# Optimization experiments

Measured on AMD Instinct MI355X. Metric: run time of the kernel, lower is better.

Reference implementation:

```python
import jax, jax.numpy as jnp
from jax import lax
import numpy as np

NA, NC = 3, 1
CONF_THRESH, IOU_THRESH = 0.5, 0.5


def _conv(x, w, b, pad):
    y = lax.conv_general_dilated(x, w, (1, 1), [(pad, pad), (pad, pad)],
                                 dimension_numbers=('NCHW', 'OIHW', 'NCHW'))
    return y + b[None, :, None, None]


def _maxpool2(x):
    return lax.reduce_window(x, -jnp.inf, lax.max, (1, 1, 2, 2), (1, 1, 2, 2), 'VALID')


def _stream(x, w1, b1, w2, b2):
    x = _maxpool2(jax.nn.relu(_conv(x, w1, b1, 1)))
    x = _maxpool2(jax.nn.relu(_conv(x, w2, b2, 1)))
    return x


def _pairwise_iou(b):
    # b: [N,4] in (x1,y1,x2,y2); matches torchvision box_iou (no area clamp)
    x1, y1, x2, y2 = b[:, 0], b[:, 1], b[:, 2], b[:, 3]
    area = (x2 - x1) * (y2 - y1)
    ix1 = jnp.maximum(x1[:, None], x1[None, :])
    iy1 = jnp.maximum(y1[:, None], y1[None, :])
    ix2 = jnp.minimum(x2[:, None], x2[None, :])
    iy2 = jnp.minimum(y2[:, None], y2[None, :])
    inter = jnp.clip(ix2 - ix1, 0.0) * jnp.clip(iy2 - iy1, 0.0)
    return inter / (area[:, None] + area[None, :] - inter)


def _nms_keep(boxes, scores, conf_keep, iou_thresh):
    # Greedy NMS over a fixed, small N; returns bool keep mask (conf + NMS).
    n = boxes.shape[0]
    order = jnp.argsort(-jnp.where(conf_keep, scores, -jnp.inf))
    iou = _pairwise_iou(boxes[order])  # [N,N] in score order
    idx = jnp.arange(n)

    def body(i, state):
        keep, suppressed = state
        valid = jnp.logical_not(suppressed[i])
        keep = keep.at[i].set(valid)
        suppressed = suppressed | (valid & (iou[i] > iou_thresh) & (idx > i))
        return keep, suppressed

    keep_sorted, _ = lax.fori_loop(0, n, body,
                                   (jnp.zeros(n, bool), jnp.zeros(n, bool)))
    keep = jnp.zeros(n, bool).at[order].set(keep_sorted)
    return keep & conf_keep


def setup_inputs() -> dict:
    key = jax.random.key(0)
    ks = jax.random.split(key, 14)
    s = 0.05
    inp = {
        'x': jax.random.normal(ks[0], (8, 3, 512, 512), jnp.float32),
        'rgb_w1': jax.random.normal(ks[1], (32, 3, 3, 3), jnp.float32) * s,
        'rgb_b1': jnp.zeros((32,), jnp.float32),
        'rgb_w2': jax.random.normal(ks[2], (64, 32, 3, 3), jnp.float32) * s,
        'rgb_b2': jnp.zeros((64,), jnp.float32),
        'ir_w1': jax.random.normal(ks[3], (32, 3, 3, 3), jnp.float32) * s,
        'ir_b1': jnp.zeros((32,), jnp.float32),
        'ir_w2': jax.random.normal(ks[4], (64, 32, 3, 3), jnp.float32) * s,
        'ir_b2': jnp.zeros((64,), jnp.float32),
        'fuse_w': jax.random.normal(ks[5], (128, 128, 3, 3), jnp.float32) * s,
        'fuse_b': jnp.zeros((128,), jnp.float32),
        'det_w': jax.random.normal(ks[6], (NA * (5 + NC), 128, 1, 1), jnp.float32),
        'det_b': jax.random.normal(ks[7], (NA * (5 + NC),), jnp.float32),
    }
    return inp


def reference(x, rgb_w1, rgb_b1, rgb_w2, rgb_b2,
              ir_w1, ir_b1, ir_w2, ir_b2,
              fuse_w, fuse_b, det_w, det_b):
    f1 = _stream(x, rgb_w1, rgb_b1, rgb_w2, rgb_b2)   # [B,64,H/4,W/4]
    f2 = _stream(x, ir_w1, ir_b1, ir_w2, ir_b2)       # [B,64,H/4,W/4]
    f = jnp.concatenate([f1, f2], axis=1)             # [B,128,H/4,W/4]
    f = jax.nn.relu(_conv(f, fuse_w, fuse_b, 1))
    f = jnp.mean(f, axis=(2, 3), keepdims=True)       # AdaptiveAvgPool2d((1,1))
    p = _conv(f, det_w, det_b, 0)                     # [B,18,1,1]
    B, C, H, W = p.shape
    p = p.reshape(B, NA, 5 + NC, H, W).transpose(0, 1, 3, 4, 2)  # [B,na,H,W,5+nc]
    boxes = p[..., :4].reshape(B, -1, 4)              # [B, na*H*W, 4]
    scores = jax.nn.sigmoid(p[..., 4]).reshape(B, -1) # [B, na*H*W]
    conf_keep = scores > CONF_THRESH
    keep = jax.vmap(_nms_keep, in_axes=(0, 0, 0, None))(boxes, scores, conf_keep,
                                                        IOU_THRESH)
    # Fixed-shape equivalent of the per-image variable-length preds list:
    # preds[b] == boxes[b][keep[b]].
    return p, boxes, scores, keep
```

## Files before the change

kernel.cpp:

```cpp
#include <hip/hip_runtime.h>
#include <math.h>


typedef __bf16 bf16x8 __attribute__((ext_vector_type(8)));
typedef float f32x4 __attribute__((ext_vector_type(4)));

static __device__ __forceinline__ ushort f2bf(float f) {
    unsigned u = __float_as_uint(f);
    unsigned r = (u + 0x7fffu + ((u >> 16) & 1u)) >> 16;
    return (ushort)r;
}
static __device__ __forceinline__ float bf2f(ushort h) {
    return __uint_as_float(((unsigned)h) << 16);
}

__global__ __launch_bounds__(256) void w1prep(
    const float* __restrict__ w_rgb, const float* __restrict__ w_ir,
    uint* __restrict__ W1p)
{
    int i = blockIdx.x * 256 + threadIdx.x;
    if (i >= 2048) return;
    int s = i >> 10, r = i & 1023;
    int oc = r >> 5, k = r & 31;
    const float* w = s ? w_ir : w_rgb;
    float v = (k < 27) ? w[oc * 27 + k] : 0.f;
    ushort h = f2bf(v);
    W1p[i] = (uint)h | ((uint)f2bf(v - bf2f(h)) << 16);
}

__global__ __launch_bounds__(256) void conv1_mfma(
    const float* __restrict__ x, const uint* __restrict__ W1p,
    const float* __restrict__ bias, ushort* __restrict__ C1h,
    ushort* __restrict__ C1l)
{
    __shared__ uint S[3 * 4 * 132];
    __shared__ float pool[4][32][32];

    const int seg = blockIdx.x, Y = blockIdx.y, b = blockIdx.z;
    const int tid = threadIdx.x, wsub = tid >> 6, lane = tid & 63;
    const int n = lane & 15, q = lane >> 4;

    uint4 bu0a = *(const uint4*)&W1p[n * 32 + q * 8];
    uint4 bu0b = *(const uint4*)&W1p[n * 32 + q * 8 + 4];
    uint4 bu1a = *(const uint4*)&W1p[(16 + n) * 32 + q * 8];
    uint4 bu1b = *(const uint4*)&W1p[(16 + n) * 32 + q * 8 + 4];

    const int ih0 = 2 * Y - 1, iw0 = seg * 128 - 1;
    for (int i = tid; i < 1584; i += 256) {
        int c = i / 528, rem = i - c * 528;
        int r = rem / 132, cc = rem - r * 132;
        int ih = ih0 + r, iw = iw0 + cc;
        float v = 0.f;
        if (cc < 130 && ih >= 0 && ih < 512 && iw >= 0 && iw < 512)
            v = x[((b * 3 + c) * 512 + ih) * 512 + iw];
        ushort h = f2bf(v);
        S[i] = (uint)h | ((uint)f2bf(v - bf2f(h)) << 16);
    }

    uint4 bh0v, bl0v, bh1v, bl1v;
    {
        uint u0[8], u1[8];
        *(uint4*)&u0[0] = bu0a; *(uint4*)&u0[4] = bu0b;
        *(uint4*)&u1[0] = bu1a; *(uint4*)&u1[4] = bu1b;
        uint* bh0 = (uint*)&bh0v; uint* bl0 = (uint*)&bl0v;
        uint* bh1 = (uint*)&bh1v; uint* bl1 = (uint*)&bl1v;
#pragma unroll
        for (int j = 0; j < 4; ++j) {
            bh0[j] = (u0[2 * j] & 0xffffu) | (u0[2 * j + 1] << 16);
            bl0[j] = (u0[2 * j] >> 16) | (u0[2 * j + 1] & 0xffff0000u);
            bh1[j] = (u1[2 * j] & 0xffffu) | (u1[2 * j + 1] << 16);
            bl1[j] = (u1[2 * j] >> 16) | (u1[2 * j + 1] & 0xffff0000u);
        }
    }
    bf16x8 Bh0 = __builtin_bit_cast(bf16x8, bh0v);
    bf16x8 Bl0 = __builtin_bit_cast(bf16x8, bl0v);
    bf16x8 Bh1 = __builtin_bit_cast(bf16x8, bh1v);
    bf16x8 Bl1 = __builtin_bit_cast(bf16x8, bl1v);

    int idx[8];
    const int off0 = (wsub & 1) * 132 + (wsub >> 1) * 64 + n;
#pragma unroll
    for (int e = 0; e < 8; ++e) {
        int k = q * 8 + e;
        int c = (k >= 18) ? ((k >= 27) ? 3 : 2) : ((k >= 9) ? 1 : 0);
        int t = k - c * 9;
        int ky = (t >= 6) ? 2 : ((t >= 3) ? 1 : 0);
        int kx = t - ky * 3;
        idx[e] = (k < 27) ? ((c * 4 + ky) * 132 + kx + off0) : 0;
    }
    __syncthreads();

    f32x4 acc[4][2];
#pragma unroll
    for (int mt = 0; mt < 4; ++mt)
#pragma unroll
        for (int nt = 0; nt < 2; ++nt) acc[mt][nt] = (f32x4){0.f, 0.f, 0.f, 0.f};

#pragma unroll
    for (int mt = 0; mt < 4; ++mt) {
        uint u[8];
#pragma unroll
        for (int e = 0; e < 8; ++e) u[e] = S[idx[e] + mt * 16];
        uint4 ahv, alv;
        uint* ah = (uint*)&ahv;
        uint* al = (uint*)&alv;
#pragma unroll
        for (int j = 0; j < 4; ++j) {
            ah[j] = (u[2 * j] & 0xffffu) | (u[2 * j + 1] << 16);
            al[j] = (u[2 * j] >> 16) | (u[2 * j + 1] & 0xffff0000u);
        }
        bf16x8 Ah = __builtin_bit_cast(bf16x8, ahv);
        bf16x8 Al = __builtin_bit_cast(bf16x8, alv);
        __builtin_amdgcn_s_setprio(1);
        acc[mt][0] = __builtin_amdgcn_mfma_f32_16x16x32_bf16(Ah, Bh0, acc[mt][0], 0, 0, 0);
        acc[mt][1] = __builtin_amdgcn_mfma_f32_16x16x32_bf16(Ah, Bh1, acc[mt][1], 0, 0, 0);
        acc[mt][0] = __builtin_amdgcn_mfma_f32_16x16x32_bf16(Ah, Bl0, acc[mt][0], 0, 0, 0);
        acc[mt][1] = __builtin_amdgcn_mfma_f32_16x16x32_bf16(Ah, Bl1, acc[mt][1], 0, 0, 0);
        acc[mt][0] = __builtin_amdgcn_mfma_f32_16x16x32_bf16(Al, Bh0, acc[mt][0], 0, 0, 0);
        acc[mt][1] = __builtin_amdgcn_mfma_f32_16x16x32_bf16(Al, Bh1, acc[mt][1], 0, 0, 0);
        __builtin_amdgcn_s_setprio(0);
    }

#pragma unroll
    for (int mt = 0; mt < 4; ++mt)
#pragma unroll
        for (int nt = 0; nt < 2; ++nt) {
            int oc = nt * 16 + n;
            int plx = mt * 8 + q * 2;
            pool[wsub][plx][oc]     = fmaxf(acc[mt][nt][0], acc[mt][nt][1]);
            pool[wsub][plx + 1][oc] = fmaxf(acc[mt][nt][2], acc[mt][nt][3]);
        }
    __syncthreads();
    {
        int plx = tid >> 2, ocq = tid & 3;
        int wp = plx >> 5, pl = plx & 31;
        __attribute__((aligned(16))) ushort hb[8], lb[8];
#pragma unroll
        for (int e = 0; e < 8; ++e) {
            int oc = ocq * 8 + e;
            float v = fmaxf(pool[wp * 2][pl][oc], pool[wp * 2 + 1][pl][oc]);
            v = fmaxf(v + bias[oc], 0.f);
            ushort h = f2bf(v);
            hb[e] = h;
            lb[e] = f2bf(v - bf2f(h));
        }
        int ow = seg * 64 + plx;
        size_t base = (((size_t)((b * 256 + Y) * 256 + ow)) << 5) + ocq * 8;
        *(uint4*)(C1h + base) = *(const uint4*)hb;
        *(uint4*)(C1l + base) = *(const uint4*)lb;
    }
}

__global__ __launch_bounds__(256) void conv2_mfma(
    const ushort* __restrict__ C1h, const ushort* __restrict__ C1l,
    const float* __restrict__ w2, const float* __restrict__ bias,
    ushort* __restrict__ Ahi, ushort* __restrict__ Alo, int stream_base)
{
    __shared__ char lds[40960];
    ushort* Bh = (ushort*)lds;
    ushort* Bl = (ushort*)(lds + 20480);
    float (*pool)[32][64] = (float (*)[32][64])lds;

    const int seg = blockIdx.x, Y = blockIdx.y, b = blockIdx.z;
    const int tid = threadIdx.x, wsub = tid >> 6, lane = tid & 63;
    const int n = lane & 15, q = lane >> 4;
    const int yc = 2 * Y + (wsub & 1);
    const int wx0 = seg * 128 + (wsub >> 1) * 64;

    const uint4 zero4 = make_uint4(0u, 0u, 0u, 0u);

    auto stageB = [&](int t0, int ntap) {
        for (int i = tid; i < ntap * 2048; i += 256) {
            int t = t0 + (i >> 11), r = i & 2047;
            float v = w2[r * 9 + t];
            ushort h = f2bf(v);
            Bh[i] = h;
            Bl[i] = f2bf(v - bf2f(h));
        }
    };

    auto loadA = [&](int t, uint4* aH, uint4* aL) {
        int ky = t / 3, kx = t - ky * 3;
        int yy = yc + ky - 1;
        bool yok = (yy >= 0) & (yy < 256);
#pragma unroll
        for (int mt = 0; mt < 4; ++mt) {
            int xp = wx0 + mt * 16 + n + kx - 1;
            bool ok = yok & (xp >= 0) & (xp < 256);
            int yyc = ok ? yy : 0, xpc = ok ? xp : 0;
            size_t off = (((size_t)((b * 256 + yyc) * 256 + xpc)) << 5) + q * 8;
            aH[mt] = ok ? *(const uint4*)(C1h + off) : zero4;
            aL[mt] = ok ? *(const uint4*)(C1l + off) : zero4;
        }
    };

    f32x4 acc[4][4];
#pragma unroll
    for (int mt = 0; mt < 4; ++mt)
#pragma unroll
        for (int nt = 0; nt < 4; ++nt) acc[mt][nt] = (f32x4){0.f, 0.f, 0.f, 0.f};

    uint4 aH[4], aL[4];
    loadA(0, aH, aL);
    stageB(0, 5);
    __syncthreads();

    for (int t = 0; t < 9; ++t) {
        if (t == 5) {
            __syncthreads();
            stageB(5, 4);
            __syncthreads();
        }
        const int rel = (t < 5) ? t : t - 5;
        uint4 cH[4], cL[4];
#pragma unroll
        for (int mt = 0; mt < 4; ++mt) { cH[mt] = aH[mt]; cL[mt] = aL[mt]; }
        if (t + 1 < 9) loadA(t + 1, aH, aL);
        bf16x8 bh[4], bl[4];
#pragma unroll
        for (int nt = 0; nt < 4; ++nt) {
            int off = rel * 2048 + (nt * 16 + n) * 32 + q * 8;
            bh[nt] = __builtin_bit_cast(bf16x8, *(const uint4*)&Bh[off]);
            bl[nt] = __builtin_bit_cast(bf16x8, *(const uint4*)&Bl[off]);
        }
        __builtin_amdgcn_s_setprio(1);
#pragma unroll
        for (int mt = 0; mt < 4; ++mt) {
            bf16x8 ah = __builtin_bit_cast(bf16x8, cH[mt]);
#pragma unroll
            for (int nt = 0; nt < 4; ++nt)
                acc[mt][nt] = __builtin_amdgcn_mfma_f32_16x16x32_bf16(ah, bh[nt], acc[mt][nt], 0, 0, 0);
        }
#pragma unroll
        for (int mt = 0; mt < 4; ++mt) {
            bf16x8 ah = __builtin_bit_cast(bf16x8, cH[mt]);
#pragma unroll
            for (int nt = 0; nt < 4; ++nt)
                acc[mt][nt] = __builtin_amdgcn_mfma_f32_16x16x32_bf16(ah, bl[nt], acc[mt][nt], 0, 0, 0);
        }
#pragma unroll
        for (int mt = 0; mt < 4; ++mt) {
            bf16x8 al = __builtin_bit_cast(bf16x8, cL[mt]);
#pragma unroll
            for (int nt = 0; nt < 4; ++nt)
                acc[mt][nt] = __builtin_amdgcn_mfma_f32_16x16x32_bf16(al, bh[nt], acc[mt][nt], 0, 0, 0);
        }
        __builtin_amdgcn_s_setprio(0);
    }

    __syncthreads();

#pragma unroll
    for (int mt = 0; mt < 4; ++mt)
#pragma unroll
        for (int nt = 0; nt < 4; ++nt) {
            int oc = nt * 16 + n;
            int plx = mt * 8 + q * 2;
            pool[wsub][plx][oc]     = fmaxf(acc[mt][nt][0], acc[mt][nt][1]);
            pool[wsub][plx + 1][oc] = fmaxf(acc[mt][nt][2], acc[mt][nt][3]);
        }
    __syncthreads();

    {
        int plx = tid >> 2, ocq = tid & 3;
        int wp = plx >> 5, pl = plx & 31;
        __attribute__((aligned(16))) ushort hb[16], lb[16];
#pragma unroll
        for (int e = 0; e < 16; ++e) {
            int oc = ocq * 16 + e;
            float v = fmaxf(pool[wp * 2][pl][oc], pool[wp * 2 + 1][pl][oc]);
            v = fmaxf(v + bias[oc], 0.f);
            ushort h = f2bf(v);
            hb[e] = h;
            lb[e] = f2bf(v - bf2f(h));
        }
        int gx = seg * 64 + plx;
        int cpl = (stream_base >> 5) + (ocq >> 1);
        int cho = (ocq & 1) * 16;
        size_t base = (((size_t)(((b * 4 + cpl) * 128 + Y) * 128 + gx)) << 5) + cho;
        uint4* dh = (uint4*)(Ahi + base);
        uint4* dl = (uint4*)(Alo + base);
        dh[0] = *(const uint4*)&hb[0];
        dh[1] = *(const uint4*)&hb[8];
        dl[0] = *(const uint4*)&lb[0];
        dl[1] = *(const uint4*)&lb[8];
    }
}

__global__ __launch_bounds__(256) void wprep(
    const float* __restrict__ fw, ushort* __restrict__ Whi,
    ushort* __restrict__ Wlo)
{
    int idx = blockIdx.x * 256 + threadIdx.x;
    if (idx >= 147456) return;
    int kk = idx & 31;
    int oc = (idx >> 5) & 127;
    int ct = idx >> 12;
    int c = ct / 9, t = ct - c * 9;
    int ic = c * 32 + kk;
    int ky = t / 3, kx = t - ky * 3;
    float v = fw[((oc * 128 + ic) * 3 + ky) * 3 + kx];
    ushort h = f2bf(v);
    Whi[idx] = h;
    Wlo[idx] = f2bf(v - bf2f(h));
}

__global__ __launch_bounds__(256, 2) void fuse_mfma(
    const ushort* __restrict__ Ahi, const ushort* __restrict__ Alo,
    const ushort* __restrict__ Whi, const ushort* __restrict__ Wlo,
    const float* __restrict__ bias, float* __restrict__ featsum)
{
    __shared__ float partial[4][128];
    const int b = blockIdx.x, ypair = blockIdx.y;
    const int tid = threadIdx.x, wsub = tid >> 6, lane = tid & 63;
    const int n = lane & 15, q = lane >> 4;
    const int y = ypair * 2 + (wsub >> 1);
    const int xbase = (wsub & 1) * 64;

    f32x4 acc[4][8];
#pragma unroll
    for (int mt = 0; mt < 4; ++mt)
#pragma unroll
        for (int g = 0; g < 8; ++g) acc[mt][g] = (f32x4){0.f, 0.f, 0.f, 0.f};

    const uint4 zero4 = make_uint4(0u, 0u, 0u, 0u);

    auto loadA = [&](int tc, uint4* oh, uint4* ol) {
        int c = tc / 9, t = tc - c * 9;
        int ky = t / 3, kx = t - ky * 3;
        int yy = y + ky - 1;
        bool yok = (yy >= 0) & (yy < 128);
#pragma unroll
        for (int mt = 0; mt < 4; ++mt) {
            int xp = xbase + mt * 16 + n + kx - 1;
            bool ok = yok & (xp >= 0) & (xp < 128);
            int yyc = ok ? yy : 0, xpc = ok ? xp : 0;
            size_t aoff = (((size_t)(((b * 4 + c) * 128 + yyc) * 128 + xpc)) << 5) + q * 8;
            oh[mt] = ok ? *(const uint4*)(Ahi + aoff) : zero4;
            ol[mt] = ok ? *(const uint4*)(Alo + aoff) : zero4;
        }
    };

    uint4 pAh[4], pAl[4];
    loadA(0, pAh, pAl);

    const ushort* WhiB = Whi + n * 32 + q * 8;
    const ushort* WloB = Wlo + n * 32 + q * 8;

    uint4 nBh[4], nBl[4];
#pragma unroll
    for (int j = 0; j < 4; ++j) {
        nBh[j] = *(const uint4*)(WhiB + j * 512);
        nBl[j] = *(const uint4*)(WloB + j * 512);
    }

    for (int tc = 0; tc < 36; ++tc) {
        uint4 cAh[4], cAl[4];
#pragma unroll
        for (int mt = 0; mt < 4; ++mt) { cAh[mt] = pAh[mt]; cAl[mt] = pAl[mt]; }
        if (tc + 1 < 36) loadA(tc + 1, pAh, pAl);
#pragma unroll
        for (int g = 0; g < 8; ++g) {
            const int slot = g & 3;
            bf16x8 bh = __builtin_bit_cast(bf16x8, nBh[slot]);
            bf16x8 bl = __builtin_bit_cast(bf16x8, nBl[slot]);
            {
                size_t off = (size_t)(tc * 8 + g + 4) * 512;
                nBh[slot] = *(const uint4*)(WhiB + off);
                nBl[slot] = *(const uint4*)(WloB + off);
            }
#pragma unroll
            for (int mt = 0; mt < 4; ++mt) {
                bf16x8 ah = __builtin_bit_cast(bf16x8, cAh[mt]);
                acc[mt][g] = __builtin_amdgcn_mfma_f32_16x16x32_bf16(ah, bh, acc[mt][g], 0, 0, 0);
            }
#pragma unroll
            for (int mt = 0; mt < 4; ++mt) {
                bf16x8 ah = __builtin_bit_cast(bf16x8, cAh[mt]);
                acc[mt][g] = __builtin_amdgcn_mfma_f32_16x16x32_bf16(ah, bl, acc[mt][g], 0, 0, 0);
            }
#pragma unroll
            for (int mt = 0; mt < 4; ++mt) {
                bf16x8 al = __builtin_bit_cast(bf16x8, cAl[mt]);
                acc[mt][g] = __builtin_amdgcn_mfma_f32_16x16x32_bf16(al, bh, acc[mt][g], 0, 0, 0);
            }
        }
    }

#pragma unroll
    for (int g = 0; g < 8; ++g) {
        float bv = bias[g * 16 + n];
        float v = 0.f;
#pragma unroll
        for (int mt = 0; mt < 4; ++mt)
#pragma unroll
            for (int r = 0; r < 4; ++r) v += fmaxf(acc[mt][g][r] + bv, 0.f);
        v += __shfl_xor(v, 16);
        v += __shfl_xor(v, 32);
        if (lane < 16) partial[wsub][g * 16 + lane] = v;
    }
    __syncthreads();
    if (tid < 128) {
        float v = partial[0][tid] + partial[1][tid] + partial[2][tid] + partial[3][tid];
        atomicAdd(&featsum[b * 128 + tid], v);
    }
}

__global__ void det_nms(const float* __restrict__ featsum,
                        const float* __restrict__ dw, const float* __restrict__ db,
                        float* __restrict__ out)
{
    const int b = threadIdx.x;
    if (b >= 8) return;
    const float inv = 1.0f / 16384.0f;

    float p[18];
    for (int j = 0; j < 18; ++j) {
        float a = db[j];
        const float* wp = &dw[j * 128];
        const float* f = &featsum[b * 128];
        for (int c = 0; c < 128; ++c) a = fmaf(wp[c], f[c] * inv, a);
        p[j] = a;
    }
    for (int a = 0; a < 3; ++a)
        for (int e = 0; e < 6; ++e) out[b * 18 + a * 6 + e] = p[a * 6 + e];

    float bx[3][4], sc[3];
    bool ck[3];
    for (int a = 0; a < 3; ++a) {
        for (int k = 0; k < 4; ++k) {
            bx[a][k] = p[a * 6 + k];
            out[144 + b * 12 + a * 4 + k] = bx[a][k];
        }
        float sg = 1.f / (1.f + expf(-p[a * 6 + 4]));
        sc[a] = sg;
        ck[a] = sg > 0.5f;
        out[240 + b * 3 + a] = sg;
    }

    float key[3];
    int order[3];
    bool used[3] = {false, false, false};
    for (int a = 0; a < 3; ++a) key[a] = ck[a] ? sc[a] : -INFINITY;
    for (int i = 0; i < 3; ++i) {
        int best = -1;
        float bk = 0.f;
        for (int a = 0; a < 3; ++a) {
            if (used[a]) continue;
            if (best < 0 || key[a] > bk) { best = a; bk = key[a]; }
        }
        order[i] = best;
        used[best] = true;
    }

    float X1[3], Y1[3], X2[3], Y2[3], AR[3];
    for (int i = 0; i < 3; ++i) {
        int o = order[i];
        X1[i] = bx[o][0]; Y1[i] = bx[o][1];
        X2[i] = bx[o][2]; Y2[i] = bx[o][3];
        AR[i] = (X2[i] - X1[i]) * (Y2[i] - Y1[i]);
    }
    bool suppressed[3] = {false, false, false}, keep_s[3];
    for (int i = 0; i < 3; ++i) {
        bool valid = !suppressed[i];
        keep_s[i] = valid;
        if (valid) {
            for (int j = i + 1; j < 3; ++j) {
                float ix1 = fmaxf(X1[i], X1[j]), iy1 = fmaxf(Y1[i], Y1[j]);
                float ix2 = fminf(X2[i], X2[j]), iy2 = fminf(Y2[i], Y2[j]);
                float inter = fmaxf(ix2 - ix1, 0.f) * fmaxf(iy2 - iy1, 0.f);
                float iou = inter / (AR[i] + AR[j] - inter);
                if (iou > 0.5f) suppressed[j] = true;
            }
        }
    }
    bool keep[3];
    for (int i = 0; i < 3; ++i) keep[order[i]] = keep_s[i];
    for (int a = 0; a < 3; ++a)
        out[264 + b * 3 + a] = (keep[a] && ck[a]) ? 1.f : 0.f;
}

__global__ void zero_feat(float* __restrict__ p)
{
    int i = blockIdx.x * 256 + threadIdx.x;
    if (i < 1024) p[i] = 0.f;
}

extern "C" void kernel_launch(void* const* d_in, const int* in_sizes, int n_in,
                              void* d_out, int out_size, void* d_ws, size_t ws_size,
                              hipStream_t stream)
{
    const float* x      = (const float*)d_in[0];
    const float* rgb_w1 = (const float*)d_in[1];
    const float* rgb_b1 = (const float*)d_in[2];
    const float* rgb_w2 = (const float*)d_in[3];
    const float* rgb_b2 = (const float*)d_in[4];
    const float* ir_w1  = (const float*)d_in[5];
    const float* ir_b1  = (const float*)d_in[6];
    const float* ir_w2  = (const float*)d_in[7];
    const float* ir_b2  = (const float*)d_in[8];
    const float* fuse_w = (const float*)d_in[9];
    const float* fuse_b = (const float*)d_in[10];
    const float* det_w  = (const float*)d_in[11];
    const float* det_b  = (const float*)d_in[12];
    float* out = (float*)d_out;

    char* ws = (char*)d_ws;
    ushort* C1h  = (ushort*)(ws);
    ushort* C1l  = (ushort*)(ws + 33554432);
    ushort* Whi  = (ushort*)(ws);
    ushort* Wlo  = (ushort*)(ws + 299008);
    float*  feat = (float*)(ws + 598016);
    ushort* Ahi  = (ushort*)(ws + 67108864);
    ushort* Alo  = (ushort*)(ws + 100663296);
    uint*   W1p  = (uint*)(ws + 134209536);

    dim3 blk(256);
    hipLaunchKernelGGL(w1prep, dim3(8), blk, 0, stream, rgb_w1, ir_w1, W1p);
    hipLaunchKernelGGL(conv1_mfma, dim3(4, 256, 8), blk, 0, stream, x, W1p, rgb_b1, C1h, C1l);
    hipLaunchKernelGGL(conv2_mfma, dim3(2, 128, 8), blk, 0, stream, C1h, C1l, rgb_w2, rgb_b2, Ahi, Alo, 0);
    hipLaunchKernelGGL(conv1_mfma, dim3(4, 256, 8), blk, 0, stream, x, W1p + 1024, ir_b1, C1h, C1l);
    hipLaunchKernelGGL(conv2_mfma, dim3(2, 128, 8), blk, 0, stream, C1h, C1l, ir_w2, ir_b2, Ahi, Alo, 64);
    hipLaunchKernelGGL(wprep, dim3(576), blk, 0, stream, fuse_w, Whi, Wlo);
    hipLaunchKernelGGL(zero_feat, dim3(4), blk, 0, stream, feat);
    hipLaunchKernelGGL(fuse_mfma, dim3(8, 64), blk, 0, stream, Ahi, Alo, Whi, Wlo, fuse_b, feat);
    hipLaunchKernelGGL(det_nms, dim3(1), dim3(64), 0, stream, feat, det_w, det_b, out);
}
```

Baseline: 508.2 us.

## Stage conv2 input rows in LDS via async global_load_lds per kernel row

Conv2 now stages, for each kernel row ky, the two needed input rows (hi and lo bf16 parts, with halo columns) into LDS using direct global-to-LDS loads. The three kx taps then read shifted windows from LDS instead of issuing separate per-tap global loads into registers. Weight staging moves to three taps per ky inside the same loop. This cuts redundant global traffic across the kx taps. In exchange it uses more LDS (which may lower occupancy), adds syncs per ky, and drops the previous register prefetch overlap between taps.

```diff
diff --git a/kernel.cpp b/kernel.cpp
--- a/kernel.cpp
+++ b/kernel.cpp
@@ -12,6 +12,11 @@
 }
 static __device__ __forceinline__ float bf2f(ushort h) {
     return __uint_as_float(((unsigned)h) << 16);
+}
+static __device__ __forceinline__ void gl_lds16(const void* g, void* l) {
+    __builtin_amdgcn_global_load_lds(
+        (const __attribute__((address_space(1))) void*)g,
+        (__attribute__((address_space(3))) void*)l, 16, 0, 0);
 }
 
 __global__ __launch_bounds__(256) void w1prep(
@@ -156,96 +161,107 @@
     const float* __restrict__ w2, const float* __restrict__ bias,
     ushort* __restrict__ Ahi, ushort* __restrict__ Alo, int stream_base)
 {
-    __shared__ char lds[40960];
-    ushort* Bh = (ushort*)lds;
-    ushort* Bl = (ushort*)(lds + 20480);
+    __shared__ __attribute__((aligned(16))) char lds[58368];
+    ushort* BhL = (ushort*)(lds + 33792);
+    ushort* BlL = (ushort*)(lds + 46080);
     float (*pool)[32][64] = (float (*)[32][64])lds;
 
     const int seg = blockIdx.x, Y = blockIdx.y, b = blockIdx.z;
     const int tid = threadIdx.x, wsub = tid >> 6, lane = tid & 63;
     const int n = lane & 15, q = lane >> 4;
-    const int yc = 2 * Y + (wsub & 1);
-    const int wx0 = seg * 128 + (wsub >> 1) * 64;
+    const int rs = wsub & 1;
+    const int xs = wsub >> 1;
 
     const uint4 zero4 = make_uint4(0u, 0u, 0u, 0u);
 
-    auto stageB = [&](int t0, int ntap) {
-        for (int i = tid; i < ntap * 2048; i += 256) {
-            int t = t0 + (i >> 11), r = i & 2047;
+    f32x4 acc[4][4];
+#pragma unroll
+    for (int mt = 0; mt < 4; ++mt)
+#pragma unroll
+        for (int nt = 0; nt < 4; ++nt) acc[mt][nt] = (f32x4){0.f, 0.f, 0.f, 0.f};
+
+    for (int ky = 0; ky < 3; ++ky) {
+        if (ky) __syncthreads();
+
+        {
+            const int hl = wsub >> 1, rsS = wsub & 1;
+            const int yy = 2 * Y + rsS + ky - 1;
+            char* dstbase = lds + hl * 16896 + rsS * 8448 + 64;
+            if (yy >= 0 && yy < 256) {
+                const ushort* src = (hl ? C1l : C1h)
+                    + ((size_t)(b * 256 + yy) * 256 + seg * 128) * 32;
+                const char* s8 = (const char*)src + lane * 16;
+#pragma unroll
+                for (int j = 0; j < 8; ++j)
+                    gl_lds16(s8 + j * 1024, dstbase + j * 1024);
+            } else {
+#pragma unroll
+                for (int j = 0; j < 8; ++j)
+                    *(uint4*)(dstbase + j * 1024 + lane * 16) = zero4;
+            }
+        }
+        if (tid < 32) {
+            int combo = tid >> 3;
+            int hl = combo >> 1, rsE = combo & 1;
+            int e = (tid >> 2) & 1, part = tid & 3;
+            int yy = 2 * Y + rsE + ky - 1;
+            int xp = seg * 128 + (e ? 128 : -1);
+            uint4 v = zero4;
+            if (yy >= 0 && yy < 256 && xp >= 0 && xp < 256) {
+                const ushort* src = (hl ? C1l : C1h)
+                    + ((size_t)(b * 256 + yy) * 256 + xp) * 32 + part * 8;
+                v = *(const uint4*)src;
+            }
+            *(uint4*)(lds + hl * 16896 + rsE * 8448 + (e ? 129 * 64 : 0) + part * 16) = v;
+        }
+        for (int i = tid; i < 6144; i += 256) {
+            int t = ky * 3 + (i >> 11), r = i & 2047;
             float v = w2[r * 9 + t];
             ushort h = f2bf(v);
-            Bh[i] = h;
-            Bl[i] = f2bf(v - bf2f(h));
-        }
-    };
-
-    auto loadA = [&](int t, uint4* aH, uint4* aL) {
-        int ky = t / 3, kx = t - ky * 3;
-        int yy = yc + ky - 1;
-        bool yok = (yy >= 0) & (yy < 256);
-#pragma unroll
-        for (int mt = 0; mt < 4; ++mt) {
-            int xp = wx0 + mt * 16 + n + kx - 1;
-            bool ok = yok & (xp >= 0) & (xp < 256);
-            int yyc = ok ? yy : 0, xpc = ok ? xp : 0;
-            size_t off = (((size_t)((b * 256 + yyc) * 256 + xpc)) << 5) + q * 8;
-            aH[mt] = ok ? *(const uint4*)(C1h + off) : zero4;
-            aL[mt] = ok ? *(const uint4*)(C1l + off) : zero4;
-        }
-    };
-
-    f32x4 acc[4][4];
-#pragma unroll
-    for (int mt = 0; mt < 4; ++mt)
-#pragma unroll
-        for (int nt = 0; nt < 4; ++nt) acc[mt][nt] = (f32x4){0.f, 0.f, 0.f, 0.f};
-
-    uint4 aH[4], aL[4];
-    loadA(0, aH, aL);
-    stageB(0, 5);
-    __syncthreads();
-
-    for (int t = 0; t < 9; ++t) {
-        if (t == 5) {
-            __syncthreads();
-            stageB(5, 4);
-            __syncthreads();
-        }
-        const int rel = (t < 5) ? t : t - 5;
-        uint4 cH[4], cL[4];
-#pragma unroll
-        for (int mt = 0; mt < 4; ++mt) { cH[mt] = aH[mt]; cL[mt] = aL[mt]; }
-        if (t + 1 < 9) loadA(t + 1, aH, aL);
-        bf16x8 bh[4], bl[4];
-#pragma unroll
-        for (int nt = 0; nt < 4; ++nt) {
-            int off = rel * 2048 + (nt * 16 + n) * 32 + q * 8;
-            bh[nt] = __builtin_bit_cast(bf16x8, *(const uint4*)&Bh[off]);
-            bl[nt] = __builtin_bit_cast(bf16x8, *(const uint4*)&Bl[off]);
-        }
-        __builtin_amdgcn_s_setprio(1);
-#pragma unroll
-        for (int mt = 0; mt < 4; ++mt) {
-            bf16x8 ah = __builtin_bit_cast(bf16x8, cH[mt]);
-#pragma unroll
-            for (int nt = 0; nt < 4; ++nt)
-                acc[mt][nt] = __builtin_amdgcn_mfma_f32_16x16x32_bf16(ah, bh[nt], acc[mt][nt], 0, 0, 0);
-        }
-#pragma unroll
-        for (int mt = 0; mt < 4; ++mt) {
-            bf16x8 ah = __builtin_bit_cast(bf16x8, cH[mt]);
-#pragma unroll
-            for (int nt = 0; nt < 4; ++nt)
-                acc[mt][nt] = __builtin_amdgcn_mfma_f32_16x16x32_bf16(ah, bl[nt], acc[mt][nt], 0, 0, 0);
-        }
-#pragma unroll
-        for (int mt = 0; mt < 4; ++mt) {
-            bf16x8 al = __builtin_bit_cast(bf16x8, cL[mt]);
-#pragma unroll
-            for (int nt = 0; nt < 4; ++nt)
-                acc[mt][nt] = __builtin_amdgcn_mfma_f32_16x16x32_bf16(al, bh[nt], acc[mt][nt], 0, 0, 0);
-        }
-        __builtin_amdgcn_s_setprio(0);
+            BhL[i] = h;
+            BlL[i] = f2bf(v - bf2f(h));
+        }
+        __syncthreads();
+
+        for (int kx = 0; kx < 3; ++kx) {
+            uint4 cH[4], cL[4];
+#pragma unroll
+            for (int mt = 0; mt < 4; ++mt) {
+                int off = rs * 8448 + (xs * 64 + mt * 16 + n + kx) * 64 + q * 16;
+                cH[mt] = *(const uint4*)(lds + off);
+                cL[mt] = *(const uint4*)(lds + 16896 + off);
+            }
+            bf16x8 bh[4], bl[4];
+#pragma unroll
+            for (int nt = 0; nt < 4; ++nt) {
+                int off = kx * 2048 + (nt * 16 + n) * 32 + q * 8;
+                bh[nt] = __builtin_bit_cast(bf16x8, *(const uint4*)&BhL[off]);
+                bl[nt] = __builtin_bit_cast(bf16x8, *(const uint4*)&BlL[off]);
+            }
+            __builtin_amdgcn_s_setprio(1);
+#pragma unroll
+            for (int mt = 0; mt < 4; ++mt) {
+                bf16x8 ah = __builtin_bit_cast(bf16x8, cH[mt]);
+#pragma unroll
+                for (int nt = 0; nt < 4; ++nt)
+                    acc[mt][nt] = __builtin_amdgcn_mfma_f32_16x16x32_bf16(ah, bh[nt], acc[mt][nt], 0, 0, 0);
+            }
+#pragma unroll
+            for (int mt = 0; mt < 4; ++mt) {
+                bf16x8 ah = __builtin_bit_cast(bf16x8, cH[mt]);
+#pragma unroll
+                for (int nt = 0; nt < 4; ++nt)
+                    acc[mt][nt] = __builtin_amdgcn_mfma_f32_16x16x32_bf16(ah, bl[nt], acc[mt][nt], 0, 0, 0);
+            }
+#pragma unroll
+            for (int mt = 0; mt < 4; ++mt) {
+                bf16x8 al = __builtin_bit_cast(bf16x8, cL[mt]);
+#pragma unroll
+                for (int nt = 0; nt < 4; ++nt)
+                    acc[mt][nt] = __builtin_amdgcn_mfma_f32_16x16x32_bf16(al, bh[nt], acc[mt][nt], 0, 0, 0);
+            }
+            __builtin_amdgcn_s_setprio(0);
+        }
     }
 
     __syncthreads();
```

Result: faster. 494.8 us (-2.6%).

## Stage all conv2 weight taps at once with vectorized loads, pad pool LDS

Applied to the files above, without the earlier changes.

conv2 now loads all nine weight taps into a larger LDS buffer in one pass using float4 global reads, removing the mid-loop barrier pair and the second staging phase. The pooling scratch arrays in conv1 and conv2 gain a padding column to avoid LDS bank conflicts. The zero_feat launch is folded into wprep to save one launch. The larger LDS footprint (72 KB) may reduce how many blocks fit per CU, and the scattered LDS writes during staging may conflict.

```diff
diff --git a/kernel.cpp b/kernel.cpp
--- a/kernel.cpp
+++ b/kernel.cpp
@@ -34,7 +34,7 @@
     ushort* __restrict__ C1l)
 {
     __shared__ uint S[3 * 4 * 132];
-    __shared__ float pool[4][32][32];
+    __shared__ float pool[4][32][33];
 
     const int seg = blockIdx.x, Y = blockIdx.y, b = blockIdx.z;
     const int tid = threadIdx.x, wsub = tid >> 6, lane = tid & 63;
@@ -156,10 +156,10 @@
     const float* __restrict__ w2, const float* __restrict__ bias,
     ushort* __restrict__ Ahi, ushort* __restrict__ Alo, int stream_base)
 {
-    __shared__ char lds[40960];
+    __shared__ __attribute__((aligned(16))) char lds[73728];
     ushort* Bh = (ushort*)lds;
-    ushort* Bl = (ushort*)(lds + 20480);
-    float (*pool)[32][64] = (float (*)[32][64])lds;
+    ushort* Bl = (ushort*)(lds + 36864);
+    float (*pool)[32][65] = (float (*)[32][65])lds;
 
     const int seg = blockIdx.x, Y = blockIdx.y, b = blockIdx.z;
     const int tid = threadIdx.x, wsub = tid >> 6, lane = tid & 63;
@@ -168,16 +168,6 @@
     const int wx0 = seg * 128 + (wsub >> 1) * 64;
 
     const uint4 zero4 = make_uint4(0u, 0u, 0u, 0u);
-
-    auto stageB = [&](int t0, int ntap) {
-        for (int i = tid; i < ntap * 2048; i += 256) {
-            int t = t0 + (i >> 11), r = i & 2047;
-            float v = w2[r * 9 + t];
-            ushort h = f2bf(v);
-            Bh[i] = h;
-            Bl[i] = f2bf(v - bf2f(h));
-        }
-    };
 
     auto loadA = [&](int t, uint4* aH, uint4* aL) {
         int ky = t / 3, kx = t - ky * 3;
@@ -202,16 +192,22 @@
 
     uint4 aH[4], aL[4];
     loadA(0, aH, aL);
-    stageB(0, 5);
+
+    for (int jj = tid; jj < 4608; jj += 256) {
+        float4 w = *(const float4*)(w2 + jj * 4);
+        float wv[4] = {w.x, w.y, w.z, w.w};
+#pragma unroll
+        for (int e = 0; e < 4; ++e) {
+            int flat = jj * 4 + e;
+            int r = flat / 9, t = flat - r * 9;
+            ushort h = f2bf(wv[e]);
+            Bh[t * 2048 + r] = h;
+            Bl[t * 2048 + r] = f2bf(wv[e] - bf2f(h));
+        }
+    }
     __syncthreads();
 
     for (int t = 0; t < 9; ++t) {
-        if (t == 5) {
-            __syncthreads();
-            stageB(5, 4);
-            __syncthreads();
-        }
-        const int rel = (t < 5) ? t : t - 5;
         uint4 cH[4], cL[4];
 #pragma unroll
         for (int mt = 0; mt < 4; ++mt) { cH[mt] = aH[mt]; cL[mt] = aL[mt]; }
@@ -219,7 +215,7 @@
         bf16x8 bh[4], bl[4];
 #pragma unroll
         for (int nt = 0; nt < 4; ++nt) {
-            int off = rel * 2048 + (nt * 16 + n) * 32 + q * 8;
+            int off = t * 2048 + (nt * 16 + n) * 32 + q * 8;
             bh[nt] = __builtin_bit_cast(bf16x8, *(const uint4*)&Bh[off]);
             bl[nt] = __builtin_bit_cast(bf16x8, *(const uint4*)&Bl[off]);
         }
@@ -289,9 +285,10 @@
 
 __global__ __launch_bounds__(256) void wprep(
     const float* __restrict__ fw, ushort* __restrict__ Whi,
-    ushort* __restrict__ Wlo)
+    ushort* __restrict__ Wlo, float* __restrict__ feat)
 {
     int idx = blockIdx.x * 256 + threadIdx.x;
+    if (idx < 1024) feat[idx] = 0.f;
     if (idx >= 147456) return;
     int kk = idx & 31;
     int oc = (idx >> 5) & 127;
@@ -478,12 +475,6 @@
     for (int i = 0; i < 3; ++i) keep[order[i]] = keep_s[i];
     for (int a = 0; a < 3; ++a)
         out[264 + b * 3 + a] = (keep[a] && ck[a]) ? 1.f : 0.f;
-}
-
-__global__ void zero_feat(float* __restrict__ p)
-{
-    int i = blockIdx.x * 256 + threadIdx.x;
-    if (i < 1024) p[i] = 0.f;
 }
 
 extern "C" void kernel_launch(void* const* d_in, const int* in_sizes, int n_in,
@@ -521,8 +512,7 @@
     hipLaunchKernelGGL(conv2_mfma, dim3(2, 128, 8), blk, 0, stream, C1h, C1l, rgb_w2, rgb_b2, Ahi, Alo, 0);
     hipLaunchKernelGGL(conv1_mfma, dim3(4, 256, 8), blk, 0, stream, x, W1p + 1024, ir_b1, C1h, C1l);
     hipLaunchKernelGGL(conv2_mfma, dim3(2, 128, 8), blk, 0, stream, C1h, C1l, ir_w2, ir_b2, Ahi, Alo, 64);
-    hipLaunchKernelGGL(wprep, dim3(576), blk, 0, stream, fuse_w, Whi, Wlo);
-    hipLaunchKernelGGL(zero_feat, dim3(4), blk, 0, stream, feat);
+    hipLaunchKernelGGL(wprep, dim3(576), blk, 0, stream, fuse_w, Whi, Wlo, feat);
     hipLaunchKernelGGL(fuse_mfma, dim3(8, 64), blk, 0, stream, Ahi, Alo, Whi, Wlo, fuse_b, feat);
     hipLaunchKernelGGL(det_nms, dim3(1), dim3(64), 0, stream, feat, det_w, det_b, out);
 }
```

Result: faster. 479.3 us, median of 5 (-5.7%).
